# Kernel tuning notes

Hardware: AMD Instinct MI355X
Metric: run time of the kernel (lower is better)

## Reference

```python
import jax, jax.numpy as jnp
import numpy as np

R = 3.82843
FREQ = 1.0
ITERATIONS = 2

def activation_fn(x):
    # cosine squashing into [0,1], then two logistic-map iterations
    x = jnp.cos(x * FREQ) * 0.5 + 0.5
    for _ in range(ITERATIONS):
        x = R * x * (1.0 - x)
    return x

def setup_inputs() -> dict:
    key = jax.random.key(0)
    ks = jax.random.split(key, 9)
    N = 2097152
    x = jax.random.normal(ks[0], (N, 2), dtype=jnp.float32)
    def init_linear(kw, kb, fan_in, fan_out):
        # torch.nn.Linear default init: U(-1/sqrt(fan_in), 1/sqrt(fan_in))
        bound = 1.0 / np.sqrt(fan_in)
        W = jax.random.uniform(kw, (fan_out, fan_in), minval=-bound, maxval=bound, dtype=jnp.float32)
        b = jax.random.uniform(kb, (fan_out,), minval=-bound, maxval=bound, dtype=jnp.float32)
        return W, b
    W1, b1 = init_linear(ks[1], ks[2], 2, 64)
    W2, b2 = init_linear(ks[3], ks[4], 64, 64)
    W3, b3 = init_linear(ks[5], ks[6], 64, 64)
    W4, b4 = init_linear(ks[7], ks[8], 64, 1)
    return {"x": x, "W1": W1, "b1": b1, "W2": W2, "b2": b2,
            "W3": W3, "b3": b3, "W4": W4, "b4": b4}

def reference(x, W1, b1, W2, b2, W3, b3, W4, b4):
    h = activation_fn(x @ W1.T + b1)   # [N, 64]
    h = activation_fn(h @ W2.T + b2)   # [N, 64]
    h = activation_fn(h @ W3.T + b3)   # [N, 64]
    out = activation_fn(h @ W4.T + b4) # [N, 1]
    return out
```

## Files before the change

kernel.cpp:

```cpp
#include <hip/hip_runtime.h>

typedef _Float16 half8  __attribute__((ext_vector_type(8)));
typedef _Float16 half4v __attribute__((ext_vector_type(4)));
typedef _Float16 half2v __attribute__((ext_vector_type(2)));
typedef float    floatx4 __attribute__((ext_vector_type(4)));
typedef float    float2v __attribute__((ext_vector_type(2)));

static constexpr float INV2PI = 0.15915494309189535f;
static constexpr float RLOG   = 3.82843f;

static constexpr double RD = (double)RLOG;
static constexpr float ACT_A = (float)(RD*RD/4.0 - RD*RD*RD/16.0);
static constexpr float ACT_B = (float)(-RD*RD/4.0 + RD*RD*RD/8.0);
static constexpr float ACT_D = (float)(-RD*RD*RD/16.0);

__device__ __forceinline__ float act_rev(float a) {
    float c = __builtin_amdgcn_cosf(a);
    float u = c * c;
    float t = __builtin_fmaf(ACT_D, u, ACT_B);
    return __builtin_fmaf(u, t, ACT_A);
}

__device__ __forceinline__ half8 act8(floatx4 a, floatx4 b) {
    float2v c0 = { __builtin_amdgcn_cosf(a[0]), __builtin_amdgcn_cosf(a[1]) };
    float2v c1 = { __builtin_amdgcn_cosf(a[2]), __builtin_amdgcn_cosf(a[3]) };
    float2v c2 = { __builtin_amdgcn_cosf(b[0]), __builtin_amdgcn_cosf(b[1]) };
    float2v c3 = { __builtin_amdgcn_cosf(b[2]), __builtin_amdgcn_cosf(b[3]) };
    float2v u0 = c0*c0, u1 = c1*c1, u2 = c2*c2, u3 = c3*c3;
    float2v t0 = __builtin_elementwise_fma(u0, (float2v)(ACT_D), (float2v)(ACT_B));
    float2v t1 = __builtin_elementwise_fma(u1, (float2v)(ACT_D), (float2v)(ACT_B));
    float2v t2 = __builtin_elementwise_fma(u2, (float2v)(ACT_D), (float2v)(ACT_B));
    float2v t3 = __builtin_elementwise_fma(u3, (float2v)(ACT_D), (float2v)(ACT_B));
    float2v h0 = __builtin_elementwise_fma(u0, t0, (float2v)(ACT_A));
    float2v h1 = __builtin_elementwise_fma(u1, t1, (float2v)(ACT_A));
    float2v h2 = __builtin_elementwise_fma(u2, t2, (float2v)(ACT_A));
    float2v h3 = __builtin_elementwise_fma(u3, t3, (float2v)(ACT_A));
    half2v e0 = __builtin_bit_cast(half2v, __builtin_amdgcn_cvt_pkrtz(h0.x, h0.y));
    half2v e1 = __builtin_bit_cast(half2v, __builtin_amdgcn_cvt_pkrtz(h1.x, h1.y));
    half2v e2 = __builtin_bit_cast(half2v, __builtin_amdgcn_cvt_pkrtz(h2.x, h2.y));
    half2v e3 = __builtin_bit_cast(half2v, __builtin_amdgcn_cvt_pkrtz(h3.x, h3.y));
    half4v lo = __builtin_shufflevector(e0, e1, 0, 1, 2, 3);
    half4v hi = __builtin_shufflevector(e2, e3, 0, 1, 2, 3);
    return __builtin_shufflevector(lo, hi, 0, 1, 2, 3, 4, 5, 6, 7);
}

struct SMem {
    half8   w2[8][64];
    half8   w3[8][64];
    floatx4 b2[4][64];
    floatx4 b3[4][64];
};

__global__ __launch_bounds__(512, 8) void mlp_fused(
    const float* __restrict__ x,
    const float* __restrict__ W1, const float* __restrict__ b1,
    const float* __restrict__ W2, const float* __restrict__ b2,
    const float* __restrict__ W3, const float* __restrict__ b3,
    const float* __restrict__ W4, const float* __restrict__ b4,
    float* __restrict__ out, int N)
{
    __shared__ SMem sm;
    const int lane = threadIdx.x & 63;
    const int wib  = threadIdx.x >> 6;
    const int m    = lane & 15;
    const int q    = lane >> 4;
    const float s  = INV2PI;
    const floatx4 zero4 = {0.0f, 0.0f, 0.0f, 0.0f};

    half8 w1f[4];
    #pragma unroll
    for (int t = 0; t < 4; ++t) {
        half8 v = {};
        if (q == 0) {
            const int n = 16 * t + m;
            float w0 = W1[2*n] * s, w1 = W1[2*n+1] * s, bb = b1[n] * s;
            _Float16 w0h = (_Float16)w0; float w0l = w0 - (float)w0h;
            _Float16 w1h = (_Float16)w1; float w1l = w1 - (float)w1h;
            _Float16 bh  = (_Float16)bb; float bl  = bb - (float)bh;
            v[0] = w0h; v[1] = w0h; v[2] = (_Float16)w0l;
            v[3] = w1h; v[4] = w1h; v[5] = (_Float16)w1l;
            v[6] = bh;  v[7] = (_Float16)bl;
        }
        w1f[t] = v;
    }
    half8 w4f[2] = {half8{}, half8{}};
    if (m == 0) {
        #pragma unroll
        for (int c = 0; c < 2; ++c)
            #pragma unroll
            for (int j = 0; j < 8; ++j) {
                int nu = (j < 4) ? (16 * c + 4 * q + j) : (16 * (c + 2) + 4 * q + j - 4);
                w4f[c][j] = (_Float16)(W4[nu] * s);
            }
    }
    floatx4 a4init = zero4;
    if (q == 0) a4init[0] = b4[0] * s;

    if (wib == 0) {
        #pragma unroll
        for (int t = 0; t < 4; ++t) {
            const float* r2 = W2 + (16 * t + m) * 64;
            #pragma unroll
            for (int c = 0; c < 2; ++c) {
                floatx4 lo2 = *(const floatx4*)(r2 + 16 * c + 4 * q);
                floatx4 hi2 = *(const floatx4*)(r2 + 16 * (c + 2) + 4 * q);
                half8 v2;
                #pragma unroll
                for (int j = 0; j < 4; ++j) {
                    v2[j]     = (_Float16)(lo2[j] * s);
                    v2[4 + j] = (_Float16)(hi2[j] * s);
                }
                sm.w2[t * 2 + c][lane] = v2;
            }
        }
    } else if (wib == 1) {
        #pragma unroll
        for (int t = 0; t < 4; ++t) {
            const float* r3 = W3 + (16 * t + m) * 64;
            #pragma unroll
            for (int c = 0; c < 2; ++c) {
                floatx4 lo3 = *(const floatx4*)(r3 + 16 * c + 4 * q);
                floatx4 hi3 = *(const floatx4*)(r3 + 16 * (c + 2) + 4 * q);
                half8 v3;
                #pragma unroll
                for (int j = 0; j < 4; ++j) {
                    v3[j]     = (_Float16)(lo3[j] * s);
                    v3[4 + j] = (_Float16)(hi3[j] * s);
                }
                sm.w3[t * 2 + c][lane] = v3;
            }
        }
    } else if (wib == 2) {
        #pragma unroll
        for (int t = 0; t < 4; ++t) {
            sm.b2[t][lane] = *(const floatx4*)(b2 + 16 * t + 4 * q) * s;
            sm.b3[t][lane] = *(const floatx4*)(b3 + 16 * t + 4 * q) * s;
        }
    }
    __syncthreads();

    const int ntiles = N >> 4;
    const int nwaves = (gridDim.x * blockDim.x) >> 6;
    const int gwave  = (int)(blockIdx.x * blockDim.x + threadIdx.x) >> 6;
    const float2* __restrict__ x2 = (const float2*)x;

    int tile = gwave;
    float2 xv = x2[(tile << 4) + m];
    while (tile < ntiles) {
        const int nt = tile + nwaves;
        float2 xnext;
        if (nt < ntiles) xnext = x2[(nt << 4) + m];

        half8 xa = {};
        if (q == 0) {
            _Float16 xh = (_Float16)xv.x; float xl = xv.x - (float)xh;
            _Float16 yh = (_Float16)xv.y; float yl = xv.y - (float)yh;
            xa[0] = xh; xa[1] = (_Float16)xl; xa[2] = xh;
            xa[3] = yh; xa[4] = (_Float16)yl; xa[5] = yh;
            xa[6] = (_Float16)1.0f; xa[7] = (_Float16)1.0f;
        }

        floatx4 a0 = __builtin_amdgcn_mfma_f32_16x16x32_f16(w1f[0], xa, zero4, 0, 0, 0);
        floatx4 a1 = __builtin_amdgcn_mfma_f32_16x16x32_f16(w1f[1], xa, zero4, 0, 0, 0);
        floatx4 a2 = __builtin_amdgcn_mfma_f32_16x16x32_f16(w1f[2], xa, zero4, 0, 0, 0);
        floatx4 a3 = __builtin_amdgcn_mfma_f32_16x16x32_f16(w1f[3], xa, zero4, 0, 0, 0);
        half8 B0 = act8(a0, a2);
        half8 B1 = act8(a1, a3);

        int z2 = 0; asm volatile("" : "+v"(z2));
        const int l2i = lane + z2;
        a0 = __builtin_amdgcn_mfma_f32_16x16x32_f16(sm.w2[0][l2i], B0, sm.b2[0][l2i], 0, 0, 0);
        a1 = __builtin_amdgcn_mfma_f32_16x16x32_f16(sm.w2[2][l2i], B0, sm.b2[1][l2i], 0, 0, 0);
        a2 = __builtin_amdgcn_mfma_f32_16x16x32_f16(sm.w2[4][l2i], B0, sm.b2[2][l2i], 0, 0, 0);
        a3 = __builtin_amdgcn_mfma_f32_16x16x32_f16(sm.w2[6][l2i], B0, sm.b2[3][l2i], 0, 0, 0);
        a0 = __builtin_amdgcn_mfma_f32_16x16x32_f16(sm.w2[1][l2i], B1, a0, 0, 0, 0);
        a1 = __builtin_amdgcn_mfma_f32_16x16x32_f16(sm.w2[3][l2i], B1, a1, 0, 0, 0);
        a2 = __builtin_amdgcn_mfma_f32_16x16x32_f16(sm.w2[5][l2i], B1, a2, 0, 0, 0);
        a3 = __builtin_amdgcn_mfma_f32_16x16x32_f16(sm.w2[7][l2i], B1, a3, 0, 0, 0);
        half8 C0 = act8(a0, a2);
        half8 C1 = act8(a1, a3);

        int z3 = 0; asm volatile("" : "+v"(z3));
        const int l3i = lane + z3;
        a0 = __builtin_amdgcn_mfma_f32_16x16x32_f16(sm.w3[0][l3i], C0, sm.b3[0][l3i], 0, 0, 0);
        a1 = __builtin_amdgcn_mfma_f32_16x16x32_f16(sm.w3[2][l3i], C0, sm.b3[1][l3i], 0, 0, 0);
        a2 = __builtin_amdgcn_mfma_f32_16x16x32_f16(sm.w3[4][l3i], C0, sm.b3[2][l3i], 0, 0, 0);
        a3 = __builtin_amdgcn_mfma_f32_16x16x32_f16(sm.w3[6][l3i], C0, sm.b3[3][l3i], 0, 0, 0);
        a0 = __builtin_amdgcn_mfma_f32_16x16x32_f16(sm.w3[1][l3i], C1, a0, 0, 0, 0);
        a1 = __builtin_amdgcn_mfma_f32_16x16x32_f16(sm.w3[3][l3i], C1, a1, 0, 0, 0);
        a2 = __builtin_amdgcn_mfma_f32_16x16x32_f16(sm.w3[5][l3i], C1, a2, 0, 0, 0);
        a3 = __builtin_amdgcn_mfma_f32_16x16x32_f16(sm.w3[7][l3i], C1, a3, 0, 0, 0);
        half8 D0 = act8(a0, a2);
        half8 D1 = act8(a1, a3);

        floatx4 a4 = __builtin_amdgcn_mfma_f32_16x16x32_f16(w4f[0], D0, a4init, 0, 0, 0);
        a4 = __builtin_amdgcn_mfma_f32_16x16x32_f16(w4f[1], D1, a4, 0, 0, 0);
        if (q == 0)
            out[(tile << 4) + m] = act_rev(a4[0]);

        xv = xnext;
        tile = nt;
    }
}

extern "C" void kernel_launch(void* const* d_in, const int* in_sizes, int n_in,
                              void* d_out, int out_size, void* d_ws, size_t ws_size,
                              hipStream_t stream) {
    const float* x  = (const float*)d_in[0];
    const float* W1 = (const float*)d_in[1];
    const float* b1 = (const float*)d_in[2];
    const float* W2 = (const float*)d_in[3];
    const float* b2 = (const float*)d_in[4];
    const float* W3 = (const float*)d_in[5];
    const float* b3 = (const float*)d_in[6];
    const float* W4 = (const float*)d_in[7];
    const float* b4 = (const float*)d_in[8];
    float* out = (float*)d_out;
    const int N = out_size;

    mlp_fused<<<dim3(1024), dim3(512), 0, stream>>>(x, W1, b1, W2, b2, W3, b3, W4, b4, out, N);
}
```

Baseline: 160.6 us.

## Process two 16-row tiles per wave iteration and retune launch geometry

```diff
diff --git a/kernel.cpp b/kernel.cpp
--- a/kernel.cpp
+++ b/kernel.cpp
@@ -51,7 +51,7 @@
     floatx4 b3[4][64];
 };
 
-__global__ __launch_bounds__(512, 8) void mlp_fused(
+__global__ __launch_bounds__(256, 5) void mlp_fused(
     const float* __restrict__ x,
     const float* __restrict__ W1, const float* __restrict__ b1,
     const float* __restrict__ W2, const float* __restrict__ b2,
@@ -139,67 +139,93 @@
     }
     __syncthreads();
 
-    const int ntiles = N >> 4;
+    const int npairs = N >> 5;
     const int nwaves = (gridDim.x * blockDim.x) >> 6;
     const int gwave  = (int)(blockIdx.x * blockDim.x + threadIdx.x) >> 6;
     const float2* __restrict__ x2 = (const float2*)x;
 
-    int tile = gwave;
-    float2 xv = x2[(tile << 4) + m];
-    while (tile < ntiles) {
-        const int nt = tile + nwaves;
-        float2 xnext;
-        if (nt < ntiles) xnext = x2[(nt << 4) + m];
-
-        half8 xa = {};
+    int pair = gwave;
+    float2 xv0 = x2[(pair << 5) + m];
+    float2 xv1 = x2[(pair << 5) + 16 + m];
+    while (pair < npairs) {
+        const int np = pair + nwaves;
+        float2 xn0, xn1;
+        if (np < npairs) {
+            xn0 = x2[(np << 5) + m];
+            xn1 = x2[(np << 5) + 16 + m];
+        }
+
+        half8 xa[2] = {half8{}, half8{}};
         if (q == 0) {
-            _Float16 xh = (_Float16)xv.x; float xl = xv.x - (float)xh;
-            _Float16 yh = (_Float16)xv.y; float yl = xv.y - (float)yh;
-            xa[0] = xh; xa[1] = (_Float16)xl; xa[2] = xh;
-            xa[3] = yh; xa[4] = (_Float16)yl; xa[5] = yh;
-            xa[6] = (_Float16)1.0f; xa[7] = (_Float16)1.0f;
-        }
-
-        floatx4 a0 = __builtin_amdgcn_mfma_f32_16x16x32_f16(w1f[0], xa, zero4, 0, 0, 0);
-        floatx4 a1 = __builtin_amdgcn_mfma_f32_16x16x32_f16(w1f[1], xa, zero4, 0, 0, 0);
-        floatx4 a2 = __builtin_amdgcn_mfma_f32_16x16x32_f16(w1f[2], xa, zero4, 0, 0, 0);
-        floatx4 a3 = __builtin_amdgcn_mfma_f32_16x16x32_f16(w1f[3], xa, zero4, 0, 0, 0);
-        half8 B0 = act8(a0, a2);
-        half8 B1 = act8(a1, a3);
+            float2 xs[2] = {xv0, xv1};
+            #pragma unroll
+            for (int u = 0; u < 2; ++u) {
+                _Float16 xh = (_Float16)xs[u].x; float xl = xs[u].x - (float)xh;
+                _Float16 yh = (_Float16)xs[u].y; float yl = xs[u].y - (float)yh;
+                xa[u][0] = xh; xa[u][1] = (_Float16)xl; xa[u][2] = xh;
+                xa[u][3] = yh; xa[u][4] = (_Float16)yl; xa[u][5] = yh;
+                xa[u][6] = (_Float16)1.0f; xa[u][7] = (_Float16)1.0f;
+            }
+        }
+
+        half8 B0[2], B1[2];
+        #pragma unroll
+        for (int u = 0; u < 2; ++u) {
+            floatx4 a0 = __builtin_amdgcn_mfma_f32_16x16x32_f16(w1f[0], xa[u], zero4, 0, 0, 0);
+            floatx4 a1 = __builtin_amdgcn_mfma_f32_16x16x32_f16(w1f[1], xa[u], zero4, 0, 0, 0);
+            floatx4 a2 = __builtin_amdgcn_mfma_f32_16x16x32_f16(w1f[2], xa[u], zero4, 0, 0, 0);
+            floatx4 a3 = __builtin_amdgcn_mfma_f32_16x16x32_f16(w1f[3], xa[u], zero4, 0, 0, 0);
+            B0[u] = act8(a0, a2);
+            B1[u] = act8(a1, a3);
+        }
 
         int z2 = 0; asm volatile("" : "+v"(z2));
         const int l2i = lane + z2;
-        a0 = __builtin_amdgcn_mfma_f32_16x16x32_f16(sm.w2[0][l2i], B0, sm.b2[0][l2i], 0, 0, 0);
-        a1 = __builtin_amdgcn_mfma_f32_16x16x32_f16(sm.w2[2][l2i], B0, sm.b2[1][l2i], 0, 0, 0);
-        a2 = __builtin_amdgcn_mfma_f32_16x16x32_f16(sm.w2[4][l2i], B0, sm.b2[2][l2i], 0, 0, 0);
-        a3 = __builtin_amdgcn_mfma_f32_16x16x32_f16(sm.w2[6][l2i], B0, sm.b2[3][l2i], 0, 0, 0);
-        a0 = __builtin_amdgcn_mfma_f32_16x16x32_f16(sm.w2[1][l2i], B1, a0, 0, 0, 0);
-        a1 = __builtin_amdgcn_mfma_f32_16x16x32_f16(sm.w2[3][l2i], B1, a1, 0, 0, 0);
-        a2 = __builtin_amdgcn_mfma_f32_16x16x32_f16(sm.w2[5][l2i], B1, a2, 0, 0, 0);
-        a3 = __builtin_amdgcn_mfma_f32_16x16x32_f16(sm.w2[7][l2i], B1, a3, 0, 0, 0);
-        half8 C0 = act8(a0, a2);
-        half8 C1 = act8(a1, a3);
+        half8 C0[2], C1[2];
+        #pragma unroll
+        for (int u = 0; u < 2; ++u) {
+            floatx4 a0 = __builtin_amdgcn_mfma_f32_16x16x32_f16(sm.w2[0][l2i], B0[u], sm.b2[0][l2i], 0, 0, 0);
+            floatx4 a1 = __builtin_amdgcn_mfma_f32_16x16x32_f16(sm.w2[2][l2i], B0[u], sm.b2[1][l2i], 0, 0, 0);
+            floatx4 a2 = __builtin_amdgcn_mfma_f32_16x16x32_f16(sm.w2[4][l2i], B0[u], sm.b2[2][l2i], 0, 0, 0);
+            floatx4 a3 = __builtin_amdgcn_mfma_f32_16x16x32_f16(sm.w2[6][l2i], B0[u], sm.b2[3][l2i], 0, 0, 0);
+            a0 = __builtin_amdgcn_mfma_f32_16x16x32_f16(sm.w2[1][l2i], B1[u], a0, 0, 0, 0);
+            a1 = __builtin_amdgcn_mfma_f32_16x16x32_f16(sm.w2[3][l2i], B1[u], a1, 0, 0, 0);
+            a2 = __builtin_amdgcn_mfma_f32_16x16x32_f16(sm.w2[5][l2i], B1[u], a2, 0, 0, 0);
+            a3 = __builtin_amdgcn_mfma_f32_16x16x32_f16(sm.w2[7][l2i], B1[u], a3, 0, 0, 0);
+            C0[u] = act8(a0, a2);
+            C1[u] = act8(a1, a3);
+        }
 
         int z3 = 0; asm volatile("" : "+v"(z3));
         const int l3i = lane + z3;
-        a0 = __builtin_amdgcn_mfma_f32_16x16x32_f16(sm.w3[0][l3i], C0, sm.b3[0][l3i], 0, 0, 0);
-        a1 = __builtin_amdgcn_mfma_f32_16x16x32_f16(sm.w3[2][l3i], C0, sm.b3[1][l3i], 0, 0, 0);
-        a2 = __builtin_amdgcn_mfma_f32_16x16x32_f16(sm.w3[4][l3i], C0, sm.b3[2][l3i], 0, 0, 0);
-        a3 = __builtin_amdgcn_mfma_f32_16x16x32_f16(sm.w3[6][l3i], C0, sm.b3[3][l3i], 0, 0, 0);
-        a0 = __builtin_amdgcn_mfma_f32_16x16x32_f16(sm.w3[1][l3i], C1, a0, 0, 0, 0);
-        a1 = __builtin_amdgcn_mfma_f32_16x16x32_f16(sm.w3[3][l3i], C1, a1, 0, 0, 0);
-        a2 = __builtin_amdgcn_mfma_f32_16x16x32_f16(sm.w3[5][l3i], C1, a2, 0, 0, 0);
-        a3 = __builtin_amdgcn_mfma_f32_16x16x32_f16(sm.w3[7][l3i], C1, a3, 0, 0, 0);
-        half8 D0 = act8(a0, a2);
-        half8 D1 = act8(a1, a3);
-
-        floatx4 a4 = __builtin_amdgcn_mfma_f32_16x16x32_f16(w4f[0], D0, a4init, 0, 0, 0);
-        a4 = __builtin_amdgcn_mfma_f32_16x16x32_f16(w4f[1], D1, a4, 0, 0, 0);
-        if (q == 0)
-            out[(tile << 4) + m] = act_rev(a4[0]);
-
-        xv = xnext;
-        tile = nt;
+        half8 D0[2], D1[2];
+        #pragma unroll
+        for (int u = 0; u < 2; ++u) {
+            floatx4 a0 = __builtin_amdgcn_mfma_f32_16x16x32_f16(sm.w3[0][l3i], C0[u], sm.b3[0][l3i], 0, 0, 0);
+            floatx4 a1 = __builtin_amdgcn_mfma_f32_16x16x32_f16(sm.w3[2][l3i], C0[u], sm.b3[1][l3i], 0, 0, 0);
+            floatx4 a2 = __builtin_amdgcn_mfma_f32_16x16x32_f16(sm.w3[4][l3i], C0[u], sm.b3[2][l3i], 0, 0, 0);
+            floatx4 a3 = __builtin_amdgcn_mfma_f32_16x16x32_f16(sm.w3[6][l3i], C0[u], sm.b3[3][l3i], 0, 0, 0);
+            a0 = __builtin_amdgcn_mfma_f32_16x16x32_f16(sm.w3[1][l3i], C1[u], a0, 0, 0, 0);
+            a1 = __builtin_amdgcn_mfma_f32_16x16x32_f16(sm.w3[3][l3i], C1[u], a1, 0, 0, 0);
+            a2 = __builtin_amdgcn_mfma_f32_16x16x32_f16(sm.w3[5][l3i], C1[u], a2, 0, 0, 0);
+            a3 = __builtin_amdgcn_mfma_f32_16x16x32_f16(sm.w3[7][l3i], C1[u], a3, 0, 0, 0);
+            D0[u] = act8(a0, a2);
+            D1[u] = act8(a1, a3);
+        }
+
+        floatx4 a4[2];
+        #pragma unroll
+        for (int u = 0; u < 2; ++u) {
+            a4[u] = __builtin_amdgcn_mfma_f32_16x16x32_f16(w4f[0], D0[u], a4init, 0, 0, 0);
+            a4[u] = __builtin_amdgcn_mfma_f32_16x16x32_f16(w4f[1], D1[u], a4[u], 0, 0, 0);
+        }
+        if (q == 0) {
+            out[(pair << 5) + m]      = act_rev(a4[0][0]);
+            out[(pair << 5) + 16 + m] = act_rev(a4[1][0]);
+        }
+
+        xv0 = xn0; xv1 = xn1;
+        pair = np;
     }
 }
 
@@ -218,5 +244,5 @@
     float* out = (float*)d_out;
     const int N = out_size;
 
-    mlp_fused<<<dim3(1024), dim3(512), 0, stream>>>(x, W1, b1, W2, b2, W3, b3, W4, b4, out, N);
-}
+    mlp_fused<<<dim3(2560), dim3(256), 0, stream>>>(x, W1, b1, W2, b2, W3, b3, W4, b4, out, N);
+}
```

Measured after the change: 168.7 us. 1.05x slower.
